# Optimization experiments

Hardware: AMD Instinct MI355X
Metric: run time of the kernel (lower is better)

Reference implementation:

```python
import jax, jax.numpy as jnp
import numpy as np

N = 50000          # nodes
E = 400000         # edges
MUL = 32           # multiplicity per irrep
NUM_NEIGHBORS = 8.0
INV_SQRT3 = 1.0 / np.sqrt(3.0)  # w3j(1,1,0) coefficient


def setup_inputs() -> dict:
    key = jax.random.key(0)
    ks = jax.random.split(key, 20)
    inp = {
        # node_input: 32x0e (dim 32) + 32x1o (dim 96) = 128
        "node_input": jax.random.normal(ks[0], (N, 4 * MUL), jnp.float32),
        "node_attr": jnp.ones((N, 1), jnp.float32),           # 1x0e trivial attr
        "edge_src": jax.random.randint(ks[1], (E,), 0, N, jnp.int32),
        "edge_dst": jax.random.randint(ks[2], (E,), 0, N, jnp.int32),
        "edge_attr": jax.random.normal(ks[3], (E, 4), jnp.float32),   # 1x0e + 1x1o
        "edge_scalars": jax.random.normal(ks[4], (E, 16), jnp.float32),
        # FullyConnectedTensorProduct weights (uvw, node_attr has mul 1)
        "w_sc0": jax.random.normal(ks[5], (MUL, MUL), jnp.float32),
        "w_sc1": jax.random.normal(ks[6], (MUL, MUL), jnp.float32),
        "w_lin1_0": jax.random.normal(ks[7], (MUL, MUL), jnp.float32),
        "w_lin1_1": jax.random.normal(ks[8], (MUL, MUL), jnp.float32),
        # radial FC net -> per-edge TP weights (numel = 4*MUL = 128)
        "fc_w1": jax.random.normal(ks[9], (16, 64), jnp.float32),
        "fc_w2": jax.random.normal(ks[10], (64, 4 * MUL), jnp.float32),
        # lin2: irreps_mid (64x0e+64x1o) x attr -> output
        "w_lin2_0": jax.random.normal(ks[11], (2 * MUL, MUL), jnp.float32),
        "w_lin2_1": jax.random.normal(ks[12], (2 * MUL, MUL), jnp.float32),
        # alpha: irreps_mid x attr -> 0e (zero-init in original; small randn for a nontrivial test)
        "w_alpha": 0.1 * jax.random.normal(ks[13], (2 * MUL, 1), jnp.float32),
        # sc_edges: irreps_mid x edge_attr -> edge_attr
        "w_se0a": jax.random.normal(ks[14], (2 * MUL,), jnp.float32),  # mid0e x ea0e -> 0e
        "w_se0b": jax.random.normal(ks[15], (2 * MUL,), jnp.float32),  # mid1o x ea1o -> 0e
        "w_se1a": jax.random.normal(ks[16], (2 * MUL,), jnp.float32),  # mid0e x ea1o -> 1o
        "w_se1b": jax.random.normal(ks[17], (2 * MUL,), jnp.float32),  # mid1o x ea0e -> 1o
    }
    return inp


def reference(node_input, node_attr, edge_src, edge_dst, edge_attr, edge_scalars,
              w_sc0, w_sc1, w_lin1_0, w_lin1_1, fc_w1, fc_w2,
              w_lin2_0, w_lin2_1, w_alpha, w_se0a, w_se0b, w_se1a, w_se1b):
    inv_nn = 1.0 / jnp.sqrt(jnp.asarray(NUM_NEIGHBORS, node_input.dtype))
    n = node_input.shape[0]
    x0 = node_input[:, :MUL]                       # (N, 32)   32x0e
    x1 = node_input[:, MUL:].reshape(n, MUL, 3)    # (N, 32, 3) 32x1o
    a = node_attr                                  # (N, 1)
    s_in = 1.0 / np.sqrt(MUL)                      # FCTP fan-in normalization

    # self-connection: FCTP(input, attr) -> output
    sc0 = (x0 @ w_sc0) * a * s_in
    sc1 = jnp.einsum('num,uw->nwm', x1, w_sc1) * a[:, :, None] * s_in
    node_self = jnp.concatenate([sc0, sc1.reshape(n, 3 * MUL)], axis=1)  # (N, 128)

    # lin1: FCTP(input, attr) -> input irreps
    f0 = (x0 @ w_lin1_0) * a * s_in
    f1 = jnp.einsum('num,uw->nwm', x1, w_lin1_1) * a[:, :, None] * s_in

    # gather source node features per edge
    g0 = f0[edge_src]                              # (E, 32)
    g1 = f1[edge_src]                              # (E, 32, 3)
    ea0 = edge_attr[:, :1]                         # (E, 1)   1x0e
    ea1 = edge_attr[:, 1:]                         # (E, 3)   1x1o

    # radial net -> per-edge TP weights (FullyConnectedNet with sin activation)
    h = jnp.sin(edge_scalars @ fc_w1 * (1.0 / np.sqrt(16.0)))
    w = h @ fc_w2 * (1.0 / np.sqrt(64.0))          # (E, 128)
    wA, wB, wC, wD = jnp.split(w, 4, axis=1)       # each (E, 32)

    # uvu tensor product, 4 instructions
    mA = wA * g0 * ea0                                           # 0e x 0e -> 0e
    mD = wD * jnp.einsum('eum,em->eu', g1, ea1) * INV_SQRT3      # 1o x 1o -> 0e
    mB = (wB * g0)[:, :, None] * ea1[:, None, :]                 # 0e x 1o -> 1o
    mC = (wC[:, :, None] * g1) * ea0[:, :, None]                 # 1o x 0e -> 1o
    mid0 = jnp.concatenate([mA, mD], axis=1)       # (E, 64)  64x0e
    mid1 = jnp.concatenate([mB, mC], axis=1)       # (E, 64, 3) 64x1o

    # scatter-add to destination nodes
    n0 = jax.ops.segment_sum(mid0, edge_dst, num_segments=n) * inv_nn
    n1 = jax.ops.segment_sum(mid1, edge_dst, num_segments=n) * inv_nn

    s_mid = 1.0 / np.sqrt(2 * MUL)
    out0 = (n0 @ w_lin2_0) * a * s_mid
    out1 = jnp.einsum('num,uw->nwm', n1, w_lin2_1) * a[:, :, None] * s_mid
    node_conv = jnp.concatenate([out0, out1.reshape(n, 3 * MUL)], axis=1)

    # alpha gate (sc.output_mask is all ones here, so alpha = 1 - 1 + alpha*1)
    alpha = (n0 @ w_alpha) * a * s_mid             # (N, 1)
    node_conv_out = node_self + alpha * node_conv  # (N, 128)

    # sc_edges: FCTP(mid, edge_attr) -> edge_attr irreps; fan-in = 128 per output
    s_se = 1.0 / np.sqrt(4 * MUL)
    se0 = ((mid0 @ w_se0a) * ea0[:, 0]
           + jnp.einsum('eum,em,u->e', mid1, ea1, w_se0b) * INV_SQRT3) * s_se
    se1 = ((mid0 @ w_se1a)[:, None] * ea1
           + jnp.einsum('eum,u->em', mid1, w_se1b) * ea0) * s_se
    edge_conv_out = edge_attr + jnp.concatenate([se0[:, None], se1], axis=1) * inv_nn

    return node_conv_out, edge_conv_out
```

## Files before the change

kernel.cpp:

```cpp
#include <hip/hip_runtime.h>
#include <math.h>

#define N_NODES 50000
#define E_EDGES 400000
#define NPRE_BLOCKS 6250
#define NHIST_BLOCKS 1563

typedef _Float16 f16x2 __attribute__((ext_vector_type(2)));
typedef _Float16 f16x4 __attribute__((ext_vector_type(4)));
typedef _Float16 f16x8 __attribute__((ext_vector_type(8)));
typedef float    f32x4 __attribute__((ext_vector_type(4)));

static constexpr float S_IN      = 0.17677669529663687f;
static constexpr float S_MID     = 0.125f;
static constexpr float S_SE      = 0.08838834764831843f;
static constexpr float INV_NN    = 0.35355339059327373f;
static constexpr float INV_SQRT3 = 0.5773502691896258f;
static constexpr float FC1_S     = 0.25f;
static constexpr float FC2_S     = 0.125f;

__device__ inline float wave_reduce_dpp(float v) {
    int x;
    x = __builtin_amdgcn_update_dpp(0, __float_as_int(v), 0x111, 0xf, 0xf, true); v += __int_as_float(x);
    x = __builtin_amdgcn_update_dpp(0, __float_as_int(v), 0x112, 0xf, 0xf, true); v += __int_as_float(x);
    x = __builtin_amdgcn_update_dpp(0, __float_as_int(v), 0x114, 0xf, 0xf, true); v += __int_as_float(x);
    x = __builtin_amdgcn_update_dpp(0, __float_as_int(v), 0x118, 0xf, 0xf, true); v += __int_as_float(x);
    x = __builtin_amdgcn_update_dpp(0, __float_as_int(v), 0x142, 0xa, 0xf, true); v += __int_as_float(x);
    x = __builtin_amdgcn_update_dpp(0, __float_as_int(v), 0x143, 0xc, 0xf, true); v += __int_as_float(x);
    return __int_as_float(__builtin_amdgcn_readlane(__float_as_int(v), 63));
}

__global__ __launch_bounds__(256) void pre_hist_kernel(
    const float* __restrict__ node_input, const float* __restrict__ node_attr,
    const float* __restrict__ w_sc0, const float* __restrict__ w_sc1,
    const float* __restrict__ w_lin1_0, const float* __restrict__ w_lin1_1,
    float* __restrict__ out_self, float* __restrict__ ws_f,
    const int* __restrict__ edge_dst, int* __restrict__ counts)
{
    const int t = threadIdx.x;
    if (blockIdx.x >= NPRE_BLOCKS) {
        const int e = (blockIdx.x - NPRE_BLOCKS) * 256 + t;
        if (e < E_EDGES) atomicAdd(&counts[edge_dst[e]], 1);
        return;
    }
    const int n0 = blockIdx.x * 8;
    __shared__ __align__(16) float sx[8 * 128];
    __shared__ float sa[8];
    ((float4*)sx)[t] = ((const float4*)(node_input + (size_t)n0 * 128))[t];
    if (t < 8) sa[t] = node_attr[n0 + t];
    __syncthreads();

    const int half = t >> 7;
    const int idx  = t & 127;
    float wcol[32];
    int m = 0;
    if (idx < 32) {
        const float* __restrict__ W = half ? w_lin1_0 : w_sc0;
        #pragma unroll
        for (int u = 0; u < 32; ++u) wcol[u] = W[u * 32 + idx];
    } else {
        const float* __restrict__ W = half ? w_lin1_1 : w_sc1;
        const int j = idx - 32;
        const int w = j / 3; m = j % 3;
        #pragma unroll
        for (int u = 0; u < 32; ++u) wcol[u] = W[u * 32 + w];
    }
    float* __restrict__ dstp = half ? ws_f : out_self;
    #pragma unroll
    for (int k = 0; k < 8; ++k) {
        const float* x = sx + k * 128;
        float acc = 0.f;
        if (idx < 32) {
            #pragma unroll
            for (int u = 0; u < 32; ++u) acc += x[u] * wcol[u];
        } else {
            #pragma unroll
            for (int u = 0; u < 32; ++u) acc += x[32 + u * 3 + m] * wcol[u];
        }
        dstp[(size_t)(n0 + k) * 128 + idx] = acc * sa[k] * S_IN;
    }
}

__global__ __launch_bounds__(1024) void scan_block_kernel(
    const int* __restrict__ counts, int* __restrict__ cursor, int* __restrict__ bsum)
{
    __shared__ int sd[1024];
    const int t   = threadIdx.x;
    const int idx = blockIdx.x * 1024 + t;
    const int c   = (idx < N_NODES) ? counts[idx] : 0;
    sd[t] = c;
    __syncthreads();
    for (int off = 1; off < 1024; off <<= 1) {
        const int v = (t >= off) ? sd[t - off] : 0;
        __syncthreads();
        sd[t] += v;
        __syncthreads();
    }
    if (idx < N_NODES) cursor[idx] = sd[t] - c;
    if (t == 1023) bsum[blockIdx.x] = sd[1023];
}

__global__ __launch_bounds__(1024) void scan_fixup_kernel(
    int* __restrict__ cursor, const int* __restrict__ bsum)
{
    __shared__ int boff_s;
    const int t = threadIdx.x;
    if (t < 64) {
        int v = (t < (int)blockIdx.x) ? bsum[t] : 0;
        #pragma unroll
        for (int off = 32; off >= 1; off >>= 1) v += __shfl_down(v, off, 64);
        if (t == 0) boff_s = v;
    }
    __syncthreads();
    const int idx = blockIdx.x * 1024 + t;
    if (idx < N_NODES) cursor[idx] += boff_s;
}

__global__ __launch_bounds__(256) void scatter_kernel(
    const int* __restrict__ edge_dst, int* __restrict__ cursor,
    int* __restrict__ sorted_eid)
{
    const int e = blockIdx.x * 256 + threadIdx.x;
    if (e < E_EDGES) {
        const int p = atomicAdd(&cursor[edge_dst[e]], 1);
        sorted_eid[p] = e;
    }
}

__global__ __launch_bounds__(256, 4) void edge_kernel(
    const float* __restrict__ ws_f,
    const int* __restrict__ edge_src, const int* __restrict__ edge_dst,
    const float* __restrict__ edge_attr, const float* __restrict__ edge_scalars,
    const float* __restrict__ fc_w1, const float* __restrict__ fc_w2,
    const float* __restrict__ w_se0a, const float* __restrict__ w_se0b,
    const float* __restrict__ w_se1a, const float* __restrict__ w_se1b,
    const int* __restrict__ sorted_eid,
    float* __restrict__ nacc, float* __restrict__ edge_out)
{
    __shared__ __align__(16) _Float16 sArena[18944];
    __shared__ __align__(16) float sEA[64 * 4];
    __shared__ int sSRC[64];
    __shared__ int sDST[64];
    __shared__ int sEID[64];

    _Float16* __restrict__ sW2T = sArena;
    _Float16* __restrict__ sHT  = sArena + 9216;
    _Float16* __restrict__ sES  = sArena + 13824;
    _Float16* __restrict__ sW1T = sArena + 16384;

    const int t    = threadIdx.x;
    const int lane = t & 63;
    const int wv   = t >> 6;
    const int quad = lane >> 4;
    const int mm   = lane & 15;
    const int e0   = blockIdx.x * 64;

    {
        const int k = t >> 4, n4 = (t & 15) * 4;
        float4 v = ((const float4*)fc_w1)[t];
        sW1T[(n4 + 0) * 40 + k] = (_Float16)v.x;
        sW1T[(n4 + 1) * 40 + k] = (_Float16)v.y;
        sW1T[(n4 + 2) * 40 + k] = (_Float16)v.z;
        sW1T[(n4 + 3) * 40 + k] = (_Float16)v.w;
        const f16x4 z4 = {(_Float16)0.f, (_Float16)0.f, (_Float16)0.f, (_Float16)0.f};
        *(f16x4*)&sW1T[(t >> 2) * 40 + 16 + (t & 3) * 4] = z4;
    }
    #pragma unroll
    for (int i = 0; i < 8; ++i) {
        const int u = t + i * 256;
        const int k = u >> 5, c4 = (u & 31) * 4;
        float4 v = ((const float4*)fc_w2)[u];
        sW2T[(c4 + 0) * 72 + k] = (_Float16)v.x;
        sW2T[(c4 + 1) * 72 + k] = (_Float16)v.y;
        sW2T[(c4 + 2) * 72 + k] = (_Float16)v.z;
        sW2T[(c4 + 3) * 72 + k] = (_Float16)v.w;
    }
    {
        const int e = t >> 2, k4 = (t & 3) * 4;
        const int eid = sorted_eid[e0 + e];
        float4 v = ((const float4*)edge_scalars)[(size_t)eid * 4 + (t & 3)];
        f16x4 p = {(_Float16)v.x, (_Float16)v.y, (_Float16)v.z, (_Float16)v.w};
        *(f16x4*)&sES[e * 40 + k4] = p;
        const f16x4 z4 = {(_Float16)0.f, (_Float16)0.f, (_Float16)0.f, (_Float16)0.f};
        *(f16x4*)&sES[e * 40 + 16 + k4] = z4;
    }
    if (t < 64) {
        const int eid = sorted_eid[e0 + t];
        *(float4*)&sEA[t * 4] = ((const float4*)edge_attr)[eid];
        sEID[t] = eid;
    } else if (t < 128) {
        sSRC[t - 64] = edge_src[sorted_eid[e0 + (t - 64)]];
    } else if (t < 192) {
        sDST[t - 128] = edge_dst[sorted_eid[e0 + (t - 128)]];
    }
    __syncthreads();

    const int eb = wv * 16;
    {
        const f16x8 a_es = *(const f16x8*)&sES[(eb + mm) * 40 + quad * 8];
        #pragma unroll
        for (int jt = 0; jt < 4; ++jt) {
            const f16x8 b = *(const f16x8*)&sW1T[(jt * 16 + mm) * 40 + quad * 8];
            f32x4 d = {0.f, 0.f, 0.f, 0.f};
            d = __builtin_amdgcn_mfma_f32_16x16x32_f16(a_es, b, d, 0, 0, 0);
            #pragma unroll
            for (int r = 0; r < 4; ++r)
                sHT[(eb + quad * 4 + r) * 72 + jt * 16 + mm] =
                    (_Float16)__sinf(d[r] * FC1_S);
        }
    }
    __syncthreads();

    f32x4 dacc[8];
    {
        const f16x8 a_lo = *(const f16x8*)&sHT[(eb + mm) * 72 + quad * 8];
        const f16x8 a_hi = *(const f16x8*)&sHT[(eb + mm) * 72 + 32 + quad * 8];
        #pragma unroll
        for (int ct = 0; ct < 8; ++ct) {
            const f16x8 b_lo = *(const f16x8*)&sW2T[(ct * 16 + mm) * 72 + quad * 8];
            const f16x8 b_hi = *(const f16x8*)&sW2T[(ct * 16 + mm) * 72 + 32 + quad * 8];
            f32x4 d = {0.f, 0.f, 0.f, 0.f};
            d = __builtin_amdgcn_mfma_f32_16x16x32_f16(a_lo, b_lo, d, 0, 0, 0);
            d = __builtin_amdgcn_mfma_f32_16x16x32_f16(a_hi, b_hi, d, 0, 0, 0);
            dacc[ct] = d;
        }
    }
    __syncthreads();

    _Float16* __restrict__ sWt = sArena;
    {
        #pragma unroll
        for (int ct = 0; ct < 8; ++ct)
            #pragma unroll
            for (int r = 0; r < 4; ++r)
                sWt[(eb + quad * 4 + r) * 130 + ct * 16 + mm] =
                    (_Float16)(dacc[ct][r] * FC2_S);
    }
    __syncthreads();

    const float se0a = w_se0a[lane], se0b = w_se0b[lane];
    const float se1a = w_se1a[lane], se1b = w_se1b[lane];
    const bool hi = lane >= 32;
    const int  u  = lane - 32;
    const int idxA = hi ? (32 + 3 * u) : lane;
    const int idxB = hi ? (33 + 3 * u) : lane;
    const int idxC = hi ? (34 + 3 * u) : lane;
    const int col1 = hi ? (96 + u) : lane;
    const int col2 = hi ? (64 + u) : (32 + lane);

    int   cur = -1;
    float am0 = 0.f, axx = 0.f, ayy = 0.f, azz = 0.f;

    for (int b = 0; b < 4; ++b) {
        float ga[4], gb[4], gc[4];
        #pragma unroll
        for (int i = 0; i < 4; ++i) {
            const int el = wv * 16 + b * 4 + i;
            const float* fr = ws_f + (size_t)sSRC[el] * 128;
            ga[i] = fr[idxA]; gb[i] = fr[idxB]; gc[i] = fr[idxC];
        }
        #pragma unroll
        for (int i = 0; i < 4; ++i) {
            const int el  = wv * 16 + b * 4 + i;
            const int dst = sDST[el];
            const float ea0 = sEA[el * 4 + 0];
            const float e1x = sEA[el * 4 + 1];
            const float e1y = sEA[el * 4 + 2];
            const float e1z = sEA[el * 4 + 3];
            const float w1v = (float)sWt[el * 130 + col1];
            const float w2v = (float)sWt[el * 130 + col2];

            float mid0, m1x, m1y, m1z;
            if (!hi) {
                mid0 = w1v * ga[i] * ea0;
                const float wbg = w2v * ga[i];
                m1x = wbg * e1x; m1y = wbg * e1y; m1z = wbg * e1z;
            } else {
                const float dot = ga[i] * e1x + gb[i] * e1y + gc[i] * e1z;
                mid0 = w1v * dot * INV_SQRT3;
                const float wce = w2v * ea0;
                m1x = wce * ga[i]; m1y = wce * gb[i]; m1z = wce * gc[i];
            }

            if (dst != cur) {
                if (cur >= 0) {
                    float* np_ = nacc + (size_t)cur * 256;
                    atomicAdd(np_ + lane, am0);
                    atomicAdd(np_ + 64 + lane * 3 + 0, axx);
                    atomicAdd(np_ + 64 + lane * 3 + 1, ayy);
                    atomicAdd(np_ + 64 + lane * 3 + 2, azz);
                }
                cur = dst; am0 = axx = ayy = azz = 0.f;
            }
            am0 += mid0; axx += m1x; ayy += m1y; azz += m1z;

            const float dotm = m1x * e1x + m1y * e1y + m1z * e1z;
            const float s0 = wave_reduce_dpp(mid0 * se0a * ea0 + dotm * se0b * INV_SQRT3);
            const float s1 = wave_reduce_dpp(mid0 * se1a);
            const float s2 = wave_reduce_dpp(m1x * se1b);
            const float s3 = wave_reduce_dpp(m1y * se1b);
            const float s4 = wave_reduce_dpp(m1z * se1b);

            if (lane == 0) {
                float4 o;
                o.x = ea0 + s0 * S_SE * INV_NN;
                o.y = e1x + (s1 * e1x + s2 * ea0) * S_SE * INV_NN;
                o.z = e1y + (s1 * e1y + s3 * ea0) * S_SE * INV_NN;
                o.w = e1z + (s1 * e1z + s4 * ea0) * S_SE * INV_NN;
                *(float4*)&edge_out[(size_t)sEID[el] * 4] = o;
            }
        }
    }
    if (cur >= 0) {
        float* np_ = nacc + (size_t)cur * 256;
        atomicAdd(np_ + lane, am0);
        atomicAdd(np_ + 64 + lane * 3 + 0, axx);
        atomicAdd(np_ + 64 + lane * 3 + 1, ayy);
        atomicAdd(np_ + 64 + lane * 3 + 2, azz);
    }
}

__global__ __launch_bounds__(128) void node_post_kernel(
    const float* __restrict__ nacc, const float* __restrict__ node_attr,
    const float* __restrict__ w_lin2_0, const float* __restrict__ w_lin2_1,
    const float* __restrict__ w_alpha, float* __restrict__ out)
{
    const int n0 = blockIdx.x * 8, t = threadIdx.x;
    __shared__ __align__(16) float sn[8 * 256];
    __shared__ float salpha[8];
    const float4* src = (const float4*)(nacc + (size_t)n0 * 256);
    #pragma unroll
    for (int i = 0; i < 4; ++i) ((float4*)sn)[t + i * 128] = src[t + i * 128];
    __syncthreads();

    if (t < 64) {
        const float wa = w_alpha[t];
        #pragma unroll
        for (int k = 0; k < 8; ++k) {
            const float r = wave_reduce_dpp(sn[k * 256 + t] * wa);
            if (t == 0) salpha[k] = r;
        }
    }
    __syncthreads();

    float wcol[64];
    int m = 0;
    if (t < 32) {
        #pragma unroll
        for (int u = 0; u < 64; ++u) wcol[u] = w_lin2_0[u * 32 + t];
    } else {
        const int j = t - 32; const int w = j / 3; m = j % 3;
        #pragma unroll
        for (int u = 0; u < 64; ++u) wcol[u] = w_lin2_1[u * 32 + w];
    }
    #pragma unroll
    for (int k = 0; k < 8; ++k) {
        const float* s = sn + k * 256;
        float acc = 0.f;
        if (t < 32) {
            #pragma unroll
            for (int u = 0; u < 64; ++u) acc += s[u] * wcol[u];
        } else {
            #pragma unroll
            for (int u = 0; u < 64; ++u) acc += s[64 + u * 3 + m] * wcol[u];
        }
        const float a  = node_attr[n0 + k];
        const float sc = a * S_MID * INV_NN;
        const size_t o = (size_t)(n0 + k) * 128 + t;
        out[o] = out[o] + (salpha[k] * sc) * (acc * sc);
    }
}

extern "C" void kernel_launch(void* const* d_in, const int* in_sizes, int n_in,
                              void* d_out, int out_size, void* d_ws, size_t ws_size,
                              hipStream_t stream)
{
    const float* node_input   = (const float*)d_in[0];
    const float* node_attr    = (const float*)d_in[1];
    const int*   edge_src     = (const int*)d_in[2];
    const int*   edge_dst     = (const int*)d_in[3];
    const float* edge_attr    = (const float*)d_in[4];
    const float* edge_scalars = (const float*)d_in[5];
    const float* w_sc0        = (const float*)d_in[6];
    const float* w_sc1        = (const float*)d_in[7];
    const float* w_lin1_0     = (const float*)d_in[8];
    const float* w_lin1_1     = (const float*)d_in[9];
    const float* fc_w1        = (const float*)d_in[10];
    const float* fc_w2        = (const float*)d_in[11];
    const float* w_lin2_0     = (const float*)d_in[12];
    const float* w_lin2_1     = (const float*)d_in[13];
    const float* w_alpha      = (const float*)d_in[14];
    const float* w_se0a       = (const float*)d_in[15];
    const float* w_se0b       = (const float*)d_in[16];
    const float* w_se1a       = (const float*)d_in[17];
    const float* w_se1b       = (const float*)d_in[18];

    float* out      = (float*)d_out;
    float* edge_out = out + (size_t)N_NODES * 128;

    float* ws_f   = (float*)d_ws;
    float* nacc   = ws_f + (size_t)N_NODES * 128;
    int*   counts = (int*)(nacc + (size_t)N_NODES * 256);
    int*   cursor = counts + N_NODES;
    int*   sid    = cursor + N_NODES;
    int*   bsum   = sid + E_EDGES;

    hipMemsetAsync(nacc, 0,
        ((size_t)N_NODES * 256 + N_NODES) * sizeof(float), stream);

    pre_hist_kernel<<<NPRE_BLOCKS + NHIST_BLOCKS, 256, 0, stream>>>(
        node_input, node_attr, w_sc0, w_sc1, w_lin1_0, w_lin1_1, out, ws_f,
        edge_dst, counts);

    scan_block_kernel<<<49, 1024, 0, stream>>>(counts, cursor, bsum);
    scan_fixup_kernel<<<49, 1024, 0, stream>>>(cursor, bsum);
    scatter_kernel<<<(E_EDGES + 255) / 256, 256, 0, stream>>>(edge_dst, cursor, sid);

    edge_kernel<<<E_EDGES / 64, 256, 0, stream>>>(
        ws_f, edge_src, edge_dst, edge_attr, edge_scalars, fc_w1, fc_w2,
        w_se0a, w_se0b, w_se1a, w_se1b, sid, nacc, edge_out);

    node_post_kernel<<<N_NODES / 8, 128, 0, stream>>>(
        nacc, node_attr, w_lin2_0, w_lin2_1, w_alpha, out);
}
```

Baseline: 418.4 us.

## Replace per-edge wave DPP reductions with an MFMA contraction for edge outputs

Instead of five wave-wide DPP reductions per edge for the sc_edges outputs, each wave writes its per-lane mid values for four edges into shared memory as fp16 and contracts them against a small weight matrix with MFMA, then four lanes finish the edge outputs. The fc MFMAs are also transposed so results are stored as vectorized f16x4 writes with a padded stride of 136. This cuts the serial reduction work in the edge loop but adds LDS traffic and fp16 rounding of the mid values. It relies on the wave's own LDS writes and reads being ordered without a barrier.

```diff
diff --git a/kernel.cpp b/kernel.cpp
--- a/kernel.cpp
+++ b/kernel.cpp
@@ -139,14 +139,18 @@
 {
     __shared__ __align__(16) _Float16 sArena[18944];
     __shared__ __align__(16) float sEA[64 * 4];
+    __shared__ __align__(16) float sDep[4][36];
     __shared__ int sSRC[64];
     __shared__ int sDST[64];
     __shared__ int sEID[64];
 
-    _Float16* __restrict__ sW2T = sArena;
-    _Float16* __restrict__ sHT  = sArena + 9216;
-    _Float16* __restrict__ sES  = sArena + 13824;
-    _Float16* __restrict__ sW1T = sArena + 16384;
+    _Float16* __restrict__ sW2T  = sArena;
+    _Float16* __restrict__ sHT   = sArena + 9216;
+    _Float16* __restrict__ sES   = sArena + 13824;
+    _Float16* __restrict__ sW1T  = sArena + 16384;
+    _Float16* __restrict__ sWt   = sArena;
+    _Float16* __restrict__ sMidA = sArena + 8704;
+    _Float16* __restrict__ sBT   = sArena + 12928;
 
     const int t    = threadIdx.x;
     const int lane = t & 63;
@@ -196,29 +200,32 @@
     __syncthreads();
 
     const int eb = wv * 16;
-    {
-        const f16x8 a_es = *(const f16x8*)&sES[(eb + mm) * 40 + quad * 8];
+
+    {
+        const f16x8 b_es = *(const f16x8*)&sES[(eb + mm) * 40 + quad * 8];
         #pragma unroll
         for (int jt = 0; jt < 4; ++jt) {
-            const f16x8 b = *(const f16x8*)&sW1T[(jt * 16 + mm) * 40 + quad * 8];
+            const f16x8 a_w1 = *(const f16x8*)&sW1T[(jt * 16 + mm) * 40 + quad * 8];
             f32x4 d = {0.f, 0.f, 0.f, 0.f};
-            d = __builtin_amdgcn_mfma_f32_16x16x32_f16(a_es, b, d, 0, 0, 0);
-            #pragma unroll
-            for (int r = 0; r < 4; ++r)
-                sHT[(eb + quad * 4 + r) * 72 + jt * 16 + mm] =
-                    (_Float16)__sinf(d[r] * FC1_S);
+            d = __builtin_amdgcn_mfma_f32_16x16x32_f16(a_w1, b_es, d, 0, 0, 0);
+            f16x4 hv;
+            hv[0] = (_Float16)__sinf(d[0] * FC1_S);
+            hv[1] = (_Float16)__sinf(d[1] * FC1_S);
+            hv[2] = (_Float16)__sinf(d[2] * FC1_S);
+            hv[3] = (_Float16)__sinf(d[3] * FC1_S);
+            *(f16x4*)&sHT[(eb + mm) * 72 + jt * 16 + quad * 4] = hv;
         }
     }
     __syncthreads();
 
     f32x4 dacc[8];
     {
-        const f16x8 a_lo = *(const f16x8*)&sHT[(eb + mm) * 72 + quad * 8];
-        const f16x8 a_hi = *(const f16x8*)&sHT[(eb + mm) * 72 + 32 + quad * 8];
+        const f16x8 b_lo = *(const f16x8*)&sHT[(eb + mm) * 72 + quad * 8];
+        const f16x8 b_hi = *(const f16x8*)&sHT[(eb + mm) * 72 + 32 + quad * 8];
         #pragma unroll
         for (int ct = 0; ct < 8; ++ct) {
-            const f16x8 b_lo = *(const f16x8*)&sW2T[(ct * 16 + mm) * 72 + quad * 8];
-            const f16x8 b_hi = *(const f16x8*)&sW2T[(ct * 16 + mm) * 72 + 32 + quad * 8];
+            const f16x8 a_lo = *(const f16x8*)&sW2T[(ct * 16 + mm) * 72 + quad * 8];
+            const f16x8 a_hi = *(const f16x8*)&sW2T[(ct * 16 + mm) * 72 + 32 + quad * 8];
             f32x4 d = {0.f, 0.f, 0.f, 0.f};
             d = __builtin_amdgcn_mfma_f32_16x16x32_f16(a_lo, b_lo, d, 0, 0, 0);
             d = __builtin_amdgcn_mfma_f32_16x16x32_f16(a_hi, b_hi, d, 0, 0, 0);
@@ -227,19 +234,29 @@
     }
     __syncthreads();
 
-    _Float16* __restrict__ sWt = sArena;
-    {
-        #pragma unroll
-        for (int ct = 0; ct < 8; ++ct)
-            #pragma unroll
-            for (int r = 0; r < 4; ++r)
-                sWt[(eb + quad * 4 + r) * 130 + ct * 16 + mm] =
-                    (_Float16)(dacc[ct][r] * FC2_S);
-    }
-    __syncthreads();
-
-    const float se0a = w_se0a[lane], se0b = w_se0b[lane];
-    const float se1a = w_se1a[lane], se1b = w_se1b[lane];
+    {
+        #pragma unroll
+        for (int ct = 0; ct < 8; ++ct) {
+            f16x4 v;
+            v[0] = (_Float16)(dacc[ct][0] * FC2_S);
+            v[1] = (_Float16)(dacc[ct][1] * FC2_S);
+            v[2] = (_Float16)(dacc[ct][2] * FC2_S);
+            v[3] = (_Float16)(dacc[ct][3] * FC2_S);
+            *(f16x4*)&sWt[(eb + mm) * 136 + ct * 16 + quad * 4] = v;
+        }
+        const f16x8 z8 = {};
+        for (int i = t; i < 528; i += 256) *(f16x8*)&sBT[i * 8] = z8;
+    }
+    __syncthreads();
+    {
+        const int u = t & 63, p = t >> 6;
+        const float ev = (p == 0) ? w_se0a[u] : w_se1b[u];
+        const float ov = (p == 0) ? w_se1a[u] : w_se0b[u];
+        sBT[(2 * p) * 264 + 4 * u + p]     = (_Float16)ev;
+        sBT[(2 * p + 1) * 264 + 4 * u + p] = (_Float16)ov;
+    }
+    __syncthreads();
+
     const bool hi = lane >= 32;
     const int  u  = lane - 32;
     const int idxA = hi ? (32 + 3 * u) : lane;
@@ -250,25 +267,28 @@
 
     int   cur = -1;
     float am0 = 0.f, axx = 0.f, ayy = 0.f, azz = 0.f;
+    _Float16* __restrict__ myA = sMidA + wv * 1056;
+    const _Float16* __restrict__ arow = myA + (mm & 3) * 264;
+    const _Float16* __restrict__ brow = sBT + mm * 264;
 
     for (int b = 0; b < 4; ++b) {
         float ga[4], gb[4], gc[4];
         #pragma unroll
         for (int i = 0; i < 4; ++i) {
-            const int el = wv * 16 + b * 4 + i;
+            const int el = eb + b * 4 + i;
             const float* fr = ws_f + (size_t)sSRC[el] * 128;
             ga[i] = fr[idxA]; gb[i] = fr[idxB]; gc[i] = fr[idxC];
         }
         #pragma unroll
         for (int i = 0; i < 4; ++i) {
-            const int el  = wv * 16 + b * 4 + i;
+            const int el  = eb + b * 4 + i;
             const int dst = sDST[el];
             const float ea0 = sEA[el * 4 + 0];
             const float e1x = sEA[el * 4 + 1];
             const float e1y = sEA[el * 4 + 2];
             const float e1z = sEA[el * 4 + 3];
-            const float w1v = (float)sWt[el * 130 + col1];
-            const float w2v = (float)sWt[el * 130 + col2];
+            const float w1v = (float)sWt[el * 136 + col1];
+            const float w2v = (float)sWt[el * 136 + col2];
 
             float mid0, m1x, m1y, m1z;
             if (!hi) {
@@ -294,21 +314,40 @@
             }
             am0 += mid0; axx += m1x; ayy += m1y; azz += m1z;
 
-            const float dotm = m1x * e1x + m1y * e1y + m1z * e1z;
-            const float s0 = wave_reduce_dpp(mid0 * se0a * ea0 + dotm * se0b * INV_SQRT3);
-            const float s1 = wave_reduce_dpp(mid0 * se1a);
-            const float s2 = wave_reduce_dpp(m1x * se1b);
-            const float s3 = wave_reduce_dpp(m1y * se1b);
-            const float s4 = wave_reduce_dpp(m1z * se1b);
-
-            if (lane == 0) {
-                float4 o;
-                o.x = ea0 + s0 * S_SE * INV_NN;
-                o.y = e1x + (s1 * e1x + s2 * ea0) * S_SE * INV_NN;
-                o.z = e1y + (s1 * e1y + s3 * ea0) * S_SE * INV_NN;
-                o.w = e1z + (s1 * e1z + s4 * ea0) * S_SE * INV_NN;
-                *(float4*)&edge_out[(size_t)sEID[el] * 4] = o;
-            }
+            f16x4 mv;
+            mv[0] = (_Float16)mid0; mv[1] = (_Float16)m1x;
+            mv[2] = (_Float16)m1y;  mv[3] = (_Float16)m1z;
+            *(f16x4*)&myA[i * 264 + 4 * lane] = mv;
+        }
+
+        f32x4 d = {0.f, 0.f, 0.f, 0.f};
+        #pragma unroll
+        for (int ks = 0; ks < 8; ++ks) {
+            const f16x8 a  = *(const f16x8*)&arow[ks * 32 + quad * 8];
+            const f16x8 bb = *(const f16x8*)&brow[ks * 32 + quad * 8];
+            d = __builtin_amdgcn_mfma_f32_16x16x32_f16(a, bb, d, 0, 0, 0);
+        }
+        if (lane < 8) {
+            float4 f4; f4.x = d[0]; f4.y = d[1]; f4.z = d[2]; f4.w = d[3];
+            *(float4*)&sDep[wv][lane * 4] = f4;
+        }
+        if (lane < 4) {
+            const int el = eb + b * 4 + lane;
+            const float c0 = sDep[wv][ 0 + lane], c1 = sDep[wv][ 4 + lane];
+            const float c2 = sDep[wv][ 8 + lane], c3 = sDep[wv][12 + lane];
+            const float c4 = sDep[wv][16 + lane], c5 = sDep[wv][20 + lane];
+            const float c6 = sDep[wv][24 + lane], c7 = sDep[wv][28 + lane];
+            const float ea0 = sEA[el * 4 + 0];
+            const float e1x = sEA[el * 4 + 1];
+            const float e1y = sEA[el * 4 + 2];
+            const float e1z = sEA[el * 4 + 3];
+            const float s0 = c0 * ea0 + (c3 * e1x + c5 * e1y + c7 * e1z) * INV_SQRT3;
+            float4 o;
+            o.x = ea0 + s0 * S_SE * INV_NN;
+            o.y = e1x + (c1 * e1x + c2 * ea0) * S_SE * INV_NN;
+            o.z = e1y + (c1 * e1y + c4 * ea0) * S_SE * INV_NN;
+            o.w = e1z + (c1 * e1z + c6 * ea0) * S_SE * INV_NN;
+            *(float4*)&edge_out[(size_t)sEID[el] * 4] = o;
         }
     }
     if (cur >= 0) {
```

Measured after the change: 413.1 us. No clear change (-1.2%).
